# Performance work log

Hardware: AMD Instinct MI355X
Metric: run time of the kernel (lower is better)

Reference implementation:

```python
import jax, jax.numpy as jnp
import numpy as np

OUT_F = 8192
IN_F = 8192
B, T = 1, 16
ZERO_POINT = 128.0  # center the simulated fp8/int codes


def setup_inputs() -> dict:
    key = jax.random.key(0)
    k_x, k_w, k_s, k_b = jax.random.split(key, 4)
    x = jax.random.normal(k_x, (B, T, IN_F), dtype=jnp.float32)
    # simulated low-precision weight codes (stands in for fp8_data)
    w_q = jax.random.randint(k_w, (OUT_F, IN_F), 0, 256, dtype=jnp.int32)
    # per-output-channel dequant scale (small positive values)
    scale = jax.random.uniform(k_s, (OUT_F,), dtype=jnp.float32) * 0.01 + 1e-4
    bias = jax.random.normal(k_b, (OUT_F,), dtype=jnp.float32)
    return {"x": x, "w_q": w_q, "scale": scale, "bias": bias}


def reference(x, w_q, scale, bias):
    # dequantize: codes -> float, per-row scale (materializes full-precision W,
    # as the original module does before F.linear)
    w = (w_q.astype(jnp.float32) - ZERO_POINT) * scale[:, None]  # [out, in]
    # F.linear: x @ W^T + b
    out = jnp.einsum('bti,oi->bto', x, w) + bias
    return out
```

## Files before the change

### kernel.cpp

```cpp
#include <hip/hip_runtime.h>


#define IN_F   8192
#define OUT_F  8192
#define NT     16
#define BLOCK  256
#define W_O    4
#define CH_PER_BLOCK 16
#define K_CHUNK 512
#define NCHUNK (IN_F / K_CHUNK)

typedef float f32x2 __attribute__((ext_vector_type(2)));

__global__ __launch_bounds__(BLOCK, 2)
void qlin_kernel(const float* __restrict__ x,
                 const int*   __restrict__ w_q,
                 const float* __restrict__ scale,
                 const float* __restrict__ bias,
                 float* __restrict__ out)
{
    __shared__ float xs[2][NT][K_CHUNK];

    const int tid  = threadIdx.x;
    const int lane = tid & 63;
    const int wave = tid >> 6;
    const int o_base = blockIdx.x * CH_PER_BLOCK + wave * W_O;

    const int* __restrict__ wr0 = w_q + (size_t)(o_base + 0) * IN_F;
    const int* __restrict__ wr1 = w_q + (size_t)(o_base + 1) * IN_F;
    const int* __restrict__ wr2 = w_q + (size_t)(o_base + 2) * IN_F;
    const int* __restrict__ wr3 = w_q + (size_t)(o_base + 3) * IN_F;

#define STAGE(c, b)                                                          \
    {                                                                        \
        _Pragma("unroll")                                                    \
        for (int r = 0; r < 8; ++r) {                                        \
            const int f = r * 4096 + wave * 1024 + lane * 16;                \
            const int t = f >> 11;                                           \
            const char* g = (const char*)x + (size_t)t * 32768 +             \
                            (size_t)(c) * 2048 + (f & 2047);                 \
            char* l = (char*)(&xs[0][0][0]) + (b) * 32768 +                  \
                      r * 4096 + wave * 1024;                                \
            __builtin_amdgcn_global_load_lds(                                \
                (const __attribute__((address_space(1))) void*)g,            \
                (__attribute__((address_space(3))) void*)l, 16, 0, 0);       \
        }                                                                    \
    }

    f32x2 acc2[NT][2];
#pragma unroll
    for (int t = 0; t < NT; ++t) {
        acc2[t][0] = (f32x2)0.0f;
        acc2[t][1] = (f32x2)0.0f;
    }

    STAGE(0, 0)
    asm volatile("s_waitcnt vmcnt(0)" ::: "memory");
    __builtin_amdgcn_s_barrier();
    __builtin_amdgcn_sched_barrier(0);

#pragma unroll 1
    for (int c = 0; c < NCHUNK; ++c) {
        const int cur = c & 1;

        if (c + 1 < NCHUNK) STAGE(c + 1, cur ^ 1)
        __builtin_amdgcn_sched_barrier(0);

#pragma unroll
        for (int ks = 0; ks < K_CHUNK / 256; ++ks) {
            const int kl = ks * 256 + lane * 4;
            const int kg = c * K_CHUNK + kl;
            const int4 w0 = *reinterpret_cast<const int4*>(wr0 + kg);
            const int4 w1 = *reinterpret_cast<const int4*>(wr1 + kg);
            const int4 w2 = *reinterpret_cast<const int4*>(wr2 + kg);
            const int4 w3 = *reinterpret_cast<const int4*>(wr3 + kg);

            f32x2 wf[2][4];
            wf[0][0] = (f32x2){(float)(w0.x - 128), (float)(w1.x - 128)};
            wf[0][1] = (f32x2){(float)(w0.y - 128), (float)(w1.y - 128)};
            wf[0][2] = (f32x2){(float)(w0.z - 128), (float)(w1.z - 128)};
            wf[0][3] = (f32x2){(float)(w0.w - 128), (float)(w1.w - 128)};
            wf[1][0] = (f32x2){(float)(w2.x - 128), (float)(w3.x - 128)};
            wf[1][1] = (f32x2){(float)(w2.y - 128), (float)(w3.y - 128)};
            wf[1][2] = (f32x2){(float)(w2.z - 128), (float)(w3.z - 128)};
            wf[1][3] = (f32x2){(float)(w2.w - 128), (float)(w3.w - 128)};

#pragma unroll
            for (int t = 0; t < NT; ++t) {
                const float4 xv = *reinterpret_cast<const float4*>(
                    &xs[cur][t][kl]);
                acc2[t][0] += wf[0][0] * (f32x2){xv.x, xv.x};
                acc2[t][1] += wf[1][0] * (f32x2){xv.x, xv.x};
                acc2[t][0] += wf[0][1] * (f32x2){xv.y, xv.y};
                acc2[t][1] += wf[1][1] * (f32x2){xv.y, xv.y};
                acc2[t][0] += wf[0][2] * (f32x2){xv.z, xv.z};
                acc2[t][1] += wf[1][2] * (f32x2){xv.z, xv.z};
                acc2[t][0] += wf[0][3] * (f32x2){xv.w, xv.w};
                acc2[t][1] += wf[1][3] * (f32x2){xv.w, xv.w};
            }
        }

        __builtin_amdgcn_sched_barrier(0);
        __builtin_amdgcn_s_barrier();
        __builtin_amdgcn_sched_barrier(0);
    }
#undef STAGE

    float myval = 0.0f;
#pragma unroll
    for (int t = 0; t < NT; ++t) {
#pragma unroll
        for (int j = 0; j < W_O; ++j) {
            float v = acc2[t][j >> 1][j & 1];
#pragma unroll
            for (int off = 32; off > 0; off >>= 1)
                v += __shfl_xor(v, off, 64);
            if (lane == (t * W_O + j)) myval = v;
        }
    }

    const int t_o = lane >> 2;
    const int o   = o_base + (lane & 3);
    out[(size_t)t_o * OUT_F + o] = myval * scale[o] + bias[o];
}

extern "C" void kernel_launch(void* const* d_in, const int* in_sizes, int n_in,
                              void* d_out, int out_size, void* d_ws, size_t ws_size,
                              hipStream_t stream) {
    const float* x     = (const float*)d_in[0];
    const int*   w_q   = (const int*)d_in[1];
    const float* scale = (const float*)d_in[2];
    const float* bias  = (const float*)d_in[3];
    float*       out   = (float*)d_out;

    dim3 grid(OUT_F / CH_PER_BLOCK);
    dim3 block(BLOCK);
    qlin_kernel<<<grid, block, 0, stream>>>(x, w_q, scale, bias, out);
}
```

Before: 64.59 us.

## Prefetch next chunk's weight codes into registers, double-buffered with LDS staging

Weight int4 loads for the next K chunk are issued into a second register buffer alongside the async LDS staging of x, and the loop is unrolled by two so the register buffers ping-pong. A partial vmcnt wait lets the x stage complete while the weight loads stay in flight across the compute of the current chunk. This hides global weight-load latency behind FMA work, at the cost of 64 extra VGPRs of prefetch state, which may pressure occupancy under launch_bounds(256,2).

After: 190.8 us. +195.5%, slower.

```diff
diff --git a/kernel.cpp b/kernel.cpp
--- a/kernel.cpp
+++ b/kernel.cpp
@@ -26,10 +26,10 @@
     const int wave = tid >> 6;
     const int o_base = blockIdx.x * CH_PER_BLOCK + wave * W_O;
 
-    const int* __restrict__ wr0 = w_q + (size_t)(o_base + 0) * IN_F;
-    const int* __restrict__ wr1 = w_q + (size_t)(o_base + 1) * IN_F;
-    const int* __restrict__ wr2 = w_q + (size_t)(o_base + 2) * IN_F;
-    const int* __restrict__ wr3 = w_q + (size_t)(o_base + 3) * IN_F;
+    const int* wrow[W_O];
+#pragma unroll
+    for (int j = 0; j < W_O; ++j)
+        wrow[j] = w_q + (size_t)(o_base + j) * IN_F;
 
 #define STAGE(c, b)                                                          \
     {                                                                        \
@@ -47,6 +47,62 @@
         }                                                                    \
     }
 
+#define PFLOAD(P, c)                                                         \
+    {                                                                        \
+        _Pragma("unroll")                                                    \
+        for (int q = 0; q < 8; ++q) {                                        \
+            const int ks = q >> 2, j = q & 3;                                \
+            P[q] = *reinterpret_cast<const int4*>(                           \
+                wrow[j] + (c) * K_CHUNK + ks * 256 + lane * 4);              \
+        }                                                                    \
+    }
+
+#define KSTEP(P, ks, cur)                                                    \
+    {                                                                        \
+        const int4 w0 = P[(ks) * 4 + 0], w1 = P[(ks) * 4 + 1];               \
+        const int4 w2 = P[(ks) * 4 + 2], w3 = P[(ks) * 4 + 3];               \
+        f32x2 wf[2][4];                                                      \
+        wf[0][0] = (f32x2){(float)(w0.x - 128), (float)(w1.x - 128)};        \
+        wf[0][1] = (f32x2){(float)(w0.y - 128), (float)(w1.y - 128)};        \
+        wf[0][2] = (f32x2){(float)(w0.z - 128), (float)(w1.z - 128)};        \
+        wf[0][3] = (f32x2){(float)(w0.w - 128), (float)(w1.w - 128)};        \
+        wf[1][0] = (f32x2){(float)(w2.x - 128), (float)(w3.x - 128)};        \
+        wf[1][1] = (f32x2){(float)(w2.y - 128), (float)(w3.y - 128)};        \
+        wf[1][2] = (f32x2){(float)(w2.z - 128), (float)(w3.z - 128)};        \
+        wf[1][3] = (f32x2){(float)(w2.w - 128), (float)(w3.w - 128)};        \
+        _Pragma("unroll")                                                    \
+        for (int t = 0; t < NT; ++t) {                                       \
+            const float4 xv = *reinterpret_cast<const float4*>(              \
+                &xs[cur][t][(ks) * 256 + lane * 4]);                         \
+            acc2[t][0] += wf[0][0] * (f32x2){xv.x, xv.x};                    \
+            acc2[t][1] += wf[1][0] * (f32x2){xv.x, xv.x};                    \
+            acc2[t][0] += wf[0][1] * (f32x2){xv.y, xv.y};                    \
+            acc2[t][1] += wf[1][1] * (f32x2){xv.y, xv.y};                    \
+            acc2[t][0] += wf[0][2] * (f32x2){xv.z, xv.z};                    \
+            acc2[t][1] += wf[1][2] * (f32x2){xv.z, xv.z};                    \
+            acc2[t][0] += wf[0][3] * (f32x2){xv.w, xv.w};                    \
+            acc2[t][1] += wf[1][3] * (f32x2){xv.w, xv.w};                    \
+        }                                                                    \
+    }
+
+#define CHUNK(c, P_CUR, P_NXT)                                               \
+    {                                                                        \
+        if ((c) + 1 < NCHUNK) {                                              \
+            STAGE((c) + 1, ((c) & 1) ^ 1)                                    \
+            __builtin_amdgcn_sched_barrier(0);                               \
+            PFLOAD(P_NXT, (c) + 1)                                           \
+        }                                                                    \
+        __builtin_amdgcn_sched_barrier(0);                                   \
+        KSTEP(P_CUR, 0, (c) & 1)                                             \
+        KSTEP(P_CUR, 1, (c) & 1)                                             \
+        __builtin_amdgcn_sched_barrier(0);                                   \
+        if ((c) + 1 < NCHUNK) {                                              \
+            asm volatile("s_waitcnt vmcnt(8)" ::: "memory");                 \
+            __builtin_amdgcn_s_barrier();                                    \
+            __builtin_amdgcn_sched_barrier(0);                               \
+        }                                                                    \
+    }
+
     f32x2 acc2[NT][2];
 #pragma unroll
     for (int t = 0; t < NT; ++t) {
@@ -54,57 +110,26 @@
         acc2[t][1] = (f32x2)0.0f;
     }
 
+    int4 pA[8], pB[8];
+
     STAGE(0, 0)
-    asm volatile("s_waitcnt vmcnt(0)" ::: "memory");
+    __builtin_amdgcn_sched_barrier(0);
+    PFLOAD(pA, 0)
+    __builtin_amdgcn_sched_barrier(0);
+    asm volatile("s_waitcnt vmcnt(8)" ::: "memory");
     __builtin_amdgcn_s_barrier();
     __builtin_amdgcn_sched_barrier(0);
 
 #pragma unroll 1
-    for (int c = 0; c < NCHUNK; ++c) {
-        const int cur = c & 1;
+    for (int cc = 0; cc < NCHUNK; cc += 2) {
+        CHUNK(cc + 0, pA, pB)
+        CHUNK(cc + 1, pB, pA)
+    }
 
-        if (c + 1 < NCHUNK) STAGE(c + 1, cur ^ 1)
-        __builtin_amdgcn_sched_barrier(0);
-
-#pragma unroll
-        for (int ks = 0; ks < K_CHUNK / 256; ++ks) {
-            const int kl = ks * 256 + lane * 4;
-            const int kg = c * K_CHUNK + kl;
-            const int4 w0 = *reinterpret_cast<const int4*>(wr0 + kg);
-            const int4 w1 = *reinterpret_cast<const int4*>(wr1 + kg);
-            const int4 w2 = *reinterpret_cast<const int4*>(wr2 + kg);
-            const int4 w3 = *reinterpret_cast<const int4*>(wr3 + kg);
-
-            f32x2 wf[2][4];
-            wf[0][0] = (f32x2){(float)(w0.x - 128), (float)(w1.x - 128)};
-            wf[0][1] = (f32x2){(float)(w0.y - 128), (float)(w1.y - 128)};
-            wf[0][2] = (f32x2){(float)(w0.z - 128), (float)(w1.z - 128)};
-            wf[0][3] = (f32x2){(float)(w0.w - 128), (float)(w1.w - 128)};
-            wf[1][0] = (f32x2){(float)(w2.x - 128), (float)(w3.x - 128)};
-            wf[1][1] = (f32x2){(float)(w2.y - 128), (float)(w3.y - 128)};
-            wf[1][2] = (f32x2){(float)(w2.z - 128), (float)(w3.z - 128)};
-            wf[1][3] = (f32x2){(float)(w2.w - 128), (float)(w3.w - 128)};
-
-#pragma unroll
-            for (int t = 0; t < NT; ++t) {
-                const float4 xv = *reinterpret_cast<const float4*>(
-                    &xs[cur][t][kl]);
-                acc2[t][0] += wf[0][0] * (f32x2){xv.x, xv.x};
-                acc2[t][1] += wf[1][0] * (f32x2){xv.x, xv.x};
-                acc2[t][0] += wf[0][1] * (f32x2){xv.y, xv.y};
-                acc2[t][1] += wf[1][1] * (f32x2){xv.y, xv.y};
-                acc2[t][0] += wf[0][2] * (f32x2){xv.z, xv.z};
-                acc2[t][1] += wf[1][2] * (f32x2){xv.z, xv.z};
-                acc2[t][0] += wf[0][3] * (f32x2){xv.w, xv.w};
-                acc2[t][1] += wf[1][3] * (f32x2){xv.w, xv.w};
-            }
-        }
-
-        __builtin_amdgcn_sched_barrier(0);
-        __builtin_amdgcn_s_barrier();
-        __builtin_amdgcn_sched_barrier(0);
-    }
 #undef STAGE
+#undef PFLOAD
+#undef KSTEP
+#undef CHUNK
 
     float myval = 0.0f;
 #pragma unroll
```

## Double block size to 32 channels per block and stream weights nontemporally

Applied to the files above, without the earlier changes.

Doubles the block to 8 waves covering 32 output channels, so each staged x chunk in shared memory is reused by twice as many channels and the grid shrinks to one block per CU. Weight reads switch to nontemporal vector loads so the single-use weight stream does not pollute the cache. Staging of x is remapped so each wave copies a contiguous row segment, and an explicit LDS wait is added before the per-chunk barrier. The trade-off is less scheduling flexibility (one resident block per CU, larger barriers) and potential tail effects from having exactly as many blocks as CUs.

New measurement: 75.49 us. 1.17x slower.

```diff
diff --git a/kernel.cpp b/kernel.cpp
--- a/kernel.cpp
+++ b/kernel.cpp
@@ -4,15 +4,16 @@
 #define IN_F   8192
 #define OUT_F  8192
 #define NT     16
-#define BLOCK  256
+#define BLOCK  512
 #define W_O    4
-#define CH_PER_BLOCK 16
+#define CH_PER_BLOCK 32
 #define K_CHUNK 512
 #define NCHUNK (IN_F / K_CHUNK)
 
 typedef float f32x2 __attribute__((ext_vector_type(2)));
+typedef int   i4x   __attribute__((ext_vector_type(4)));
 
-__global__ __launch_bounds__(BLOCK, 2)
+__global__ __launch_bounds__(BLOCK, 1)
 void qlin_kernel(const float* __restrict__ x,
                  const int*   __restrict__ w_q,
                  const float* __restrict__ scale,
@@ -26,21 +27,21 @@
     const int wave = tid >> 6;
     const int o_base = blockIdx.x * CH_PER_BLOCK + wave * W_O;
 
-    const int* __restrict__ wr0 = w_q + (size_t)(o_base + 0) * IN_F;
-    const int* __restrict__ wr1 = w_q + (size_t)(o_base + 1) * IN_F;
-    const int* __restrict__ wr2 = w_q + (size_t)(o_base + 2) * IN_F;
-    const int* __restrict__ wr3 = w_q + (size_t)(o_base + 3) * IN_F;
+    const i4x* __restrict__ wq0 = (const i4x*)(w_q + (size_t)(o_base + 0) * IN_F);
+    const i4x* __restrict__ wq1 = (const i4x*)(w_q + (size_t)(o_base + 1) * IN_F);
+    const i4x* __restrict__ wq2 = (const i4x*)(w_q + (size_t)(o_base + 2) * IN_F);
+    const i4x* __restrict__ wq3 = (const i4x*)(w_q + (size_t)(o_base + 3) * IN_F);
 
 #define STAGE(c, b)                                                          \
     {                                                                        \
         _Pragma("unroll")                                                    \
-        for (int r = 0; r < 8; ++r) {                                        \
-            const int f = r * 4096 + wave * 1024 + lane * 16;                \
-            const int t = f >> 11;                                           \
-            const char* g = (const char*)x + (size_t)t * 32768 +             \
-                            (size_t)(c) * 2048 + (f & 2047);                 \
+        for (int r = 0; r < 4; ++r) {                                        \
+            const int row = r * 4 + (wave >> 1);                             \
+            const char* g = (const char*)x + (size_t)row * (IN_F * 4) +      \
+                            (size_t)(c) * 2048 + (wave & 1) * 1024 +         \
+                            lane * 16;                                       \
             char* l = (char*)(&xs[0][0][0]) + (b) * 32768 +                  \
-                      r * 4096 + wave * 1024;                                \
+                      r * 8192 + wave * 1024;                                \
             __builtin_amdgcn_global_load_lds(                                \
                 (const __attribute__((address_space(1))) void*)g,            \
                 (__attribute__((address_space(3))) void*)l, 16, 0, 0);       \
@@ -55,6 +56,7 @@
     }
 
     STAGE(0, 0)
+    __builtin_amdgcn_sched_barrier(0);
     asm volatile("s_waitcnt vmcnt(0)" ::: "memory");
     __builtin_amdgcn_s_barrier();
     __builtin_amdgcn_sched_barrier(0);
@@ -69,21 +71,18 @@
 #pragma unroll
         for (int ks = 0; ks < K_CHUNK / 256; ++ks) {
             const int kl = ks * 256 + lane * 4;
-            const int kg = c * K_CHUNK + kl;
-            const int4 w0 = *reinterpret_cast<const int4*>(wr0 + kg);
-            const int4 w1 = *reinterpret_cast<const int4*>(wr1 + kg);
-            const int4 w2 = *reinterpret_cast<const int4*>(wr2 + kg);
-            const int4 w3 = *reinterpret_cast<const int4*>(wr3 + kg);
+            const int kq = c * (K_CHUNK / 4) + ks * 64 + lane;
+            const i4x w0 = __builtin_nontemporal_load(wq0 + kq);
+            const i4x w1 = __builtin_nontemporal_load(wq1 + kq);
+            const i4x w2 = __builtin_nontemporal_load(wq2 + kq);
+            const i4x w3 = __builtin_nontemporal_load(wq3 + kq);
 
             f32x2 wf[2][4];
-            wf[0][0] = (f32x2){(float)(w0.x - 128), (float)(w1.x - 128)};
-            wf[0][1] = (f32x2){(float)(w0.y - 128), (float)(w1.y - 128)};
-            wf[0][2] = (f32x2){(float)(w0.z - 128), (float)(w1.z - 128)};
-            wf[0][3] = (f32x2){(float)(w0.w - 128), (float)(w1.w - 128)};
-            wf[1][0] = (f32x2){(float)(w2.x - 128), (float)(w3.x - 128)};
-            wf[1][1] = (f32x2){(float)(w2.y - 128), (float)(w3.y - 128)};
-            wf[1][2] = (f32x2){(float)(w2.z - 128), (float)(w3.z - 128)};
-            wf[1][3] = (f32x2){(float)(w2.w - 128), (float)(w3.w - 128)};
+#pragma unroll
+            for (int e = 0; e < 4; ++e) {
+                wf[0][e] = (f32x2){(float)(w0[e] - 128), (float)(w1[e] - 128)};
+                wf[1][e] = (f32x2){(float)(w2[e] - 128), (float)(w3[e] - 128)};
+            }
 
 #pragma unroll
             for (int t = 0; t < NT; ++t) {
@@ -101,6 +100,7 @@
         }
 
         __builtin_amdgcn_sched_barrier(0);
+        asm volatile("s_waitcnt lgkmcnt(0)" ::: "memory");
         __builtin_amdgcn_s_barrier();
         __builtin_amdgcn_sched_barrier(0);
     }
```
